# Kernel tuning notes

Hardware: AMD Instinct MI355X
Metric: run time of the kernel (lower is better)

Reference implementation:

```python
import jax, jax.numpy as jnp
import numpy as np

B, N, C = 4, 4096, 1024
H, M = 16, 64          # num_heads, num_landmarks
DH = C // H
SCALE = H ** (-0.5)    # faithful to source: num_heads**-0.5
LN_EPS = 1e-5


def setup_inputs() -> dict:
    key = jax.random.key(0)
    ks = jax.random.split(key, 8)
    s = 0.02
    return {
        "x": jax.random.normal(ks[0], (B, N, C), jnp.float32),
        "ln_w": jnp.ones((C,), jnp.float32),
        "ln_b": jnp.zeros((C,), jnp.float32),
        "qkv_w": jax.random.normal(ks[1], (3 * C, C), jnp.float32) * s,
        "qkv_b": jax.random.normal(ks[2], (3 * C,), jnp.float32) * s,
        "gamma_w": jax.random.normal(ks[3], (C, C), jnp.float32) * s,
        "gamma_b": jax.random.normal(ks[4], (C,), jnp.float32) * s,
        "proj_w": jax.random.normal(ks[5], (C, C), jnp.float32) * s,
        "proj_b": jax.random.normal(ks[6], (C,), jnp.float32) * s,
    }


def _iterative_inv(K, n_iter=6):
    # Newton-Schulz pseudo-inverse on [..., M, M]
    Id = jnp.eye(K.shape[-1], dtype=K.dtype)
    KA = jnp.abs(K)
    V0 = KA.sum(axis=-2, keepdims=True).max(axis=-1, keepdims=True)
    VI = KA.sum(axis=-1, keepdims=True).max(axis=-2, keepdims=True)
    V = jnp.swapaxes(K, -2, -1) / (V0 * VI)
    for _ in range(n_iter):
        KV = K @ V
        V = 0.25 * V @ (13.0 * Id - KV @ (15.0 * Id - KV @ (7.0 * Id - KV)))
    return V


def reference(x, ln_w, ln_b, qkv_w, qkv_b, gamma_w, gamma_b, proj_w, proj_b):
    # LayerNorm
    mu = x.mean(axis=-1, keepdims=True)
    var = x.var(axis=-1, keepdims=True)
    xn = (x - mu) * jax.lax.rsqrt(var + LN_EPS) * ln_w + ln_b
    # qkv: (B,N,3C) -> (3,B,H,N,DH)
    qkv = (xn @ qkv_w.T + qkv_b).reshape(B, N, 3, H, DH).transpose(2, 0, 3, 1, 4)
    q, k, v = qkv[0], qkv[1], qkv[2]
    # landmarks: mean-pool segments of length N//M, then scale
    q_lm = q.reshape(B, H, M, N // M, DH).mean(axis=-2) * SCALE  # (B,H,M,DH)
    k_lm = k.reshape(B, H, M, N // M, DH).mean(axis=-2) * SCALE
    attn1 = jax.nn.softmax(jnp.einsum('bhnd,bhmd->bhnm', q, k_lm), axis=-1)    # (B,H,N,M)
    attn2 = jax.nn.softmax(jnp.einsum('bhmd,bhld->bhml', q_lm, k_lm), axis=-1)  # (B,H,M,M)
    attn3 = jax.nn.softmax(jnp.einsum('bhmd,bhnd->bhmn', q_lm, k), axis=-1)    # (B,H,M,N)
    attn2_inv = _iterative_inv(attn2)
    out = attn1 @ (attn2_inv @ (attn3 @ v))            # (B,H,N,DH)
    out = out.transpose(0, 2, 1, 3).reshape(B, N, C)
    out = out @ gamma_w.T + gamma_b                    # LipNorm=True branch
    out = out @ proj_w.T + proj_b                      # proj (dropout p=0 is identity)
    return out
```

## Files before the change

kernel.cpp:

```cpp
#include <hip/hip_runtime.h>
#include <stdint.h>

typedef unsigned short u16;
typedef short bf16x8 __attribute__((ext_vector_type(8)));
typedef float f32x4 __attribute__((ext_vector_type(4)));

#define MFMA16(a, b, c) __builtin_amdgcn_mfma_f32_16x16x32_bf16((a), (b), (c), 0, 0, 0)

static __device__ __forceinline__ float bfu2f(u16 u) {
  union { unsigned int i; float f; } z; z.i = ((unsigned int)u) << 16; return z.f;
}
static __device__ __forceinline__ u16 f2bfu(float f) {
  union { float f; unsigned int i; } z; z.f = f;
  unsigned int i = z.i;
  return (u16)((i + 0x7fffu + ((i >> 16) & 1u)) >> 16);
}

__device__ __forceinline__ void gload_lds16(const void* g, void* l) {
  __builtin_amdgcn_global_load_lds((const __attribute__((address_space(1))) void*)g,
                                   (__attribute__((address_space(3))) void*)l, 16, 0, 0);
}

__global__ __launch_bounds__(256) void ln_kernel(
    const float* __restrict__ x, const float* __restrict__ w,
    const float* __restrict__ b, u16* __restrict__ xn) {
  int row = blockIdx.x;
  int t = threadIdx.x;
  const float4* xr = (const float4*)(x + (size_t)row * 1024);
  float4 v = xr[t];
  float s = v.x + v.y + v.z + v.w;
  float ss = v.x * v.x + v.y * v.y + v.z * v.z + v.w * v.w;
#pragma unroll
  for (int m = 1; m < 64; m <<= 1) { s += __shfl_xor(s, m); ss += __shfl_xor(ss, m); }
  __shared__ float sb[4], ssb[4];
  int lane = t & 63, wvi = t >> 6;
  if (lane == 0) { sb[wvi] = s; ssb[wvi] = ss; }
  __syncthreads();
  s = sb[0] + sb[1] + sb[2] + sb[3];
  ss = ssb[0] + ssb[1] + ssb[2] + ssb[3];
  float mu = s * (1.0f / 1024.0f);
  float var = ss * (1.0f / 1024.0f) - mu * mu;
  float rstd = rsqrtf(var + 1e-5f);
  float4 wv4 = ((const float4*)w)[t];
  float4 bv4 = ((const float4*)b)[t];
  ushort4 o;
  o.x = f2bfu((v.x - mu) * rstd * wv4.x + bv4.x);
  o.y = f2bfu((v.y - mu) * rstd * wv4.y + bv4.y);
  o.z = f2bfu((v.z - mu) * rstd * wv4.z + bv4.z);
  o.w = f2bfu((v.w - mu) * rstd * wv4.w + bv4.w);
  ((ushort4*)xn)[(size_t)row * 256 + t] = o;
}

__global__ void cvt3_kernel(const float* __restrict__ a, u16* __restrict__ oa, int na,
                            const float* __restrict__ b, u16* __restrict__ ob, int nb,
                            const float* __restrict__ c, u16* __restrict__ oc, int nc) {
  int total = (na + nb + nc) >> 2;
  for (int i = blockIdx.x * blockDim.x + threadIdx.x; i < total; i += gridDim.x * blockDim.x) {
    int j = i << 2;
    const float* s; u16* d; int off;
    if (j < na) { s = a; d = oa; off = j; }
    else if (j < na + nb) { s = b; d = ob; off = j - na; }
    else { s = c; d = oc; off = j - na - nb; }
    float4 v = *(const float4*)(s + off);
    ushort4 o;
    o.x = f2bfu(v.x); o.y = f2bfu(v.y); o.z = f2bfu(v.z); o.w = f2bfu(v.w);
    *(ushort4*)(d + off) = o;
  }
}

template <int MODE>
__global__ __launch_bounds__(512, 2) void gemm_bt(
    const u16* __restrict__ A, const u16* __restrict__ Bw,
    const float* __restrict__ bias,
    float* __restrict__ Cf, u16* __restrict__ Cb,
    u16* __restrict__ Qo, u16* __restrict__ Ko, u16* __restrict__ Vo,
    int M, int N, int K) {
  __shared__ __attribute__((aligned(16))) u16 As[2][16384];
  __shared__ __attribute__((aligned(16))) u16 Bs[2][16384];
  int tid = threadIdx.x;
  int lane = tid & 63;
  int w = tid >> 6;
  int wr = w >> 2, wc = w & 3;
  int r16 = lane & 15, hi = lane >> 4;
  int l8 = lane >> 3, li = lane & 7;

  int nwg = gridDim.x * gridDim.y;
  int flat = blockIdx.y * gridDim.x + blockIdx.x;
  int q8 = nwg >> 3;
  int swz = (flat & 7) * q8 + (flat >> 3);
  int bx = swz % gridDim.x, by = swz / gridDim.x;

  const char* Abase = (const char*)(A + (size_t)by * 256 * K);
  const char* Bbase = (const char*)(Bw + (size_t)bx * 256 * K);
  size_t rowbytes = (size_t)K * 2;
  int colsw = (li ^ l8) << 4;
  int nkt = K >> 6;

  f32x4 z4 = {0.f, 0.f, 0.f, 0.f};
  f32x4 acc[8][4];
#pragma unroll
  for (int m = 0; m < 8; ++m)
#pragma unroll
    for (int n = 0; n < 4; ++n) acc[m][n] = z4;

#define SG_A(buf, t, r0)                                                      \
  gload_lds16(Abase + (size_t)((r0) + w * 8 + l8) * rowbytes + ((t) << 7) +   \
                  colsw,                                                      \
              (char*)As[buf] + ((r0) + w * 8) * 128)
#define SG_B(buf, t, r0)                                                      \
  gload_lds16(Bbase + (size_t)((r0) + w * 8 + l8) * rowbytes + ((t) << 7) +   \
                  colsw,                                                      \
              (char*)Bs[buf] + ((r0) + w * 8) * 128)

  SG_A(0, 0, 0); SG_A(0, 0, 64); SG_A(0, 0, 128); SG_A(0, 0, 192);
  SG_B(0, 0, 0); SG_B(0, 0, 64); SG_B(0, 0, 128); SG_B(0, 0, 192);
  SG_A(1, 1, 0); SG_A(1, 1, 128); SG_B(1, 1, 0); SG_B(1, 1, 64);
  SG_A(1, 1, 64); SG_A(1, 1, 192);
  asm volatile("s_waitcnt vmcnt(6)" ::: "memory");
  __builtin_amdgcn_s_barrier();
  __builtin_amdgcn_sched_barrier(0);

  int buf = 0;
  bf16x8 af[4][2], bfr[4][2];

#define LDA(mh)                                                               \
  _Pragma("unroll") for (int m = 0; m < 4; ++m) {                             \
    int row = wr * 128 + (mh) * 64 + m * 16 + r16;                            \
    int sw = (row & 7) << 4;                                                  \
    _Pragma("unroll") for (int kk = 0; kk < 2; ++kk)                          \
        af[m][kk] = *(const bf16x8*)(ab + row * 128 +                         \
                                     (((kk << 6) | (hi << 4)) ^ sw));         \
  }
#define LDB(nh)                                                               \
  _Pragma("unroll") for (int n = 0; n < 2; ++n) {                             \
    int row = wc * 64 + (nh) * 32 + n * 16 + r16;                             \
    int sw = (row & 7) << 4;                                                  \
    _Pragma("unroll") for (int kk = 0; kk < 2; ++kk)                          \
        bfr[(nh) * 2 + n][kk] = *(const bf16x8*)(ab2 + row * 128 +            \
                                     (((kk << 6) | (hi << 4)) ^ sw));         \
  }
#define MM(mh, nh)                                                            \
  __builtin_amdgcn_s_setprio(1);                                              \
  _Pragma("unroll") for (int kk = 0; kk < 2; ++kk)                            \
      _Pragma("unroll") for (int m = 0; m < 4; ++m)                           \
          _Pragma("unroll") for (int n = 0; n < 2; ++n)                       \
              acc[(mh) * 4 + m][(nh) * 2 + n] =                               \
      MFMA16(af[m][kk], bfr[(nh) * 2 + n][kk], acc[(mh) * 4 + m][(nh) * 2 + n]); \
  __builtin_amdgcn_s_setprio(0)

#define BAR1                                                                  \
  __builtin_amdgcn_s_barrier();                                               \
  __builtin_amdgcn_sched_barrier(0)
#define BAR2                                                                  \
  __builtin_amdgcn_sched_barrier(0);                                          \
  __builtin_amdgcn_s_barrier();                                               \
  __builtin_amdgcn_sched_barrier(0)

  for (int t = 0; t < nkt; ++t) {
    const char* ab = (const char*)As[buf];
    const char* ab2 = (const char*)Bs[buf];
    bool s1 = (t + 1 < nkt), s2 = (t + 2 < nkt);
    LDA(0);
    LDB(0);
    if (s1) { SG_B(buf ^ 1, t + 1, 128); SG_B(buf ^ 1, t + 1, 192); }
    BAR1;
    MM(0, 0);
    BAR2;
    LDB(1);
    if (s2) { SG_A(buf, t + 2, 0); SG_A(buf, t + 2, 128); }
    BAR1;
    MM(0, 1);
    BAR2;
    LDA(1);
    if (s2) { SG_B(buf, t + 2, 0); SG_B(buf, t + 2, 64); }
    BAR1;
    MM(1, 0);
    BAR2;
    if (s2) { SG_A(buf, t + 2, 64); SG_A(buf, t + 2, 192); }
    BAR1;
    MM(1, 1);
    __builtin_amdgcn_sched_barrier(0);
    if (s2) {
      asm volatile("s_waitcnt vmcnt(6)" ::: "memory");
    } else {
      asm volatile("s_waitcnt vmcnt(0)" ::: "memory");
    }
    __builtin_amdgcn_s_barrier();
    __builtin_amdgcn_sched_barrier(0);
    buf ^= 1;
  }
#undef SG_A
#undef SG_B
#undef LDA
#undef LDB
#undef MM
#undef BAR1
#undef BAR2

#pragma unroll
  for (int m = 0; m < 8; ++m)
#pragma unroll
    for (int n = 0; n < 4; ++n) {
      int row0 = by * 256 + wr * 128 + m * 16 + hi * 4;
      int col = bx * 256 + wc * 64 + n * 16 + r16;
      if (MODE == 2) {
        int jt = col >> 10;
        int h = (col >> 6) & 15, dh = col & 63;
        int bb = row0 >> 12, nt0 = row0 & 4095;
        float bcol = bias[col];
        if (jt == 2) {
          ushort4 o;
          o.x = f2bfu(acc[m][n][0] + bcol);
          o.y = f2bfu(acc[m][n][1] + bcol);
          o.z = f2bfu(acc[m][n][2] + bcol);
          o.w = f2bfu(acc[m][n][3] + bcol);
          *(ushort4*)&Vo[(((size_t)bb * 16 + h) * 64 + dh) * 4096 + nt0] = o;
        } else {
          u16* dst = (jt == 0) ? Qo : Ko;
#pragma unroll
          for (int r = 0; r < 4; ++r)
            dst[(((size_t)bb * 16 + h) * 4096 + nt0 + r) * 64 + dh] =
                f2bfu(acc[m][n][r] + bcol);
        }
      } else {
        float bcol = bias[col];
#pragma unroll
        for (int r = 0; r < 4; ++r) {
          int row = row0 + r;
          float val = acc[m][n][r] + bcol;
          if (MODE == 1) Cf[(size_t)row * N + col] = val;
          else           Cb[(size_t)row * N + col] = f2bfu(val);
        }
      }
    }
}

__global__ __launch_bounds__(256) void w2_kernel(
    const u16* __restrict__ A, const u16* __restrict__ Bw,
    float* __restrict__ Cp) {
  __shared__ __attribute__((aligned(16))) u16 As[8192];
  __shared__ __attribute__((aligned(16))) u16 Bs[8192];
  int tid = threadIdx.x, lane = tid & 63, w = tid >> 6;
  int wr = w >> 1, wc = w & 1;
  int r16 = lane & 15, hi = lane >> 4;
  int l8 = lane >> 3, li = lane & 7;
  int bx = blockIdx.x, by = blockIdx.y, kz = blockIdx.z;
  const char* Abase = (const char*)(A + (size_t)by * 131072 + kz * 256);
  const char* Bbase = (const char*)(Bw + (size_t)bx * 131072 + kz * 256);
  int colsw = (li ^ l8) << 4;
  f32x4 z4 = {0.f, 0.f, 0.f, 0.f};
  f32x4 acc[4][4];
#pragma unroll
  for (int m = 0; m < 4; ++m)
#pragma unroll
    for (int n = 0; n < 4; ++n) acc[m][n] = z4;

  for (int kt = 0; kt < 4; ++kt) {
    int kb = kt << 7;
#pragma unroll
    for (int i = 0; i < 4; ++i) {
      int c = w * 4 + i;
      int rr = c * 8 + l8;
      gload_lds16(Abase + (size_t)rr * 2048 + kb + colsw, (char*)As + c * 1024);
      gload_lds16(Bbase + (size_t)rr * 2048 + kb + colsw, (char*)Bs + c * 1024);
    }
    __syncthreads();
    int sw = (lane & 7) << 4;
#pragma unroll
    for (int kk = 0; kk < 2; ++kk) {
      int kby = (kk << 6) + (hi << 4);
      bf16x8 af[4], bfr[4];
#pragma unroll
      for (int m = 0; m < 4; ++m) {
        int row = wr * 64 + m * 16 + r16;
        af[m] = *(const bf16x8*)((const char*)As + row * 128 + (kby ^ sw));
      }
#pragma unroll
      for (int n = 0; n < 4; ++n) {
        int row = wc * 64 + n * 16 + r16;
        bfr[n] = *(const bf16x8*)((const char*)Bs + row * 128 + (kby ^ sw));
      }
#pragma unroll
      for (int m = 0; m < 4; ++m)
#pragma unroll
        for (int n = 0; n < 4; ++n) acc[m][n] = MFMA16(af[m], bfr[n], acc[m][n]);
    }
    __syncthreads();
  }
#pragma unroll
  for (int m = 0; m < 4; ++m)
#pragma unroll
    for (int n = 0; n < 4; ++n)
#pragma unroll
      for (int r = 0; r < 4; ++r) {
        int row = by * 128 + wr * 64 + m * 16 + hi * 4 + r;
        int col = bx * 128 + wc * 64 + n * 16 + r16;
        Cp[(size_t)kz * 1048576 + (size_t)row * 1024 + col] = acc[m][n][r];
      }
}

__global__ __launch_bounds__(256) void w2_reduce_kernel(
    const float* __restrict__ Cp, u16* __restrict__ W2b) {
  int idx4 = blockIdx.x * 256 + threadIdx.x;
  const float4* p = (const float4*)Cp + idx4;
  float4 s = p[0];
  float4 b = p[262144], c = p[524288], d = p[786432];
  s.x += b.x + c.x + d.x;
  s.y += b.y + c.y + d.y;
  s.z += b.z + c.z + d.z;
  s.w += b.w + c.w + d.w;
  ushort4 o;
  o.x = f2bfu(s.x); o.y = f2bfu(s.y); o.z = f2bfu(s.z); o.w = f2bfu(s.w);
  ((ushort4*)W2b)[idx4] = o;
}

__global__ __launch_bounds__(64) void landmark_kernel(
    const u16* __restrict__ Q, const u16* __restrict__ K,
    float* __restrict__ qlmf, u16* __restrict__ qlmb,
    float* __restrict__ klmf, u16* __restrict__ klmb) {
  int bm = blockIdx.x;
  int bh = bm >> 6, m = bm & 63;
  int l = threadIdx.x;
  const u16* src = blockIdx.y ? K : Q;
  const u16* base = src + (((size_t)bh * 4096) + m * 64) * 64;
  int r0 = l >> 3;
  int c0 = (l & 7) * 8;
  float s[8] = {};
#pragma unroll
  for (int p = 0; p < 8; ++p) {
    bf16x8 v = *(const bf16x8*)(base + (size_t)(r0 + p * 8) * 64 + c0);
#pragma unroll
    for (int j = 0; j < 8; ++j) s[j] += bfu2f((u16)v[j]);
  }
#pragma unroll
  for (int j = 0; j < 8; ++j) {
    s[j] += __shfl_xor(s[j], 8);
    s[j] += __shfl_xor(s[j], 16);
    s[j] += __shfl_xor(s[j], 32);
  }
  if (l < 8) {
    size_t o = (size_t)bh * 4096 + m * 64 + l * 8;
    float* fo = blockIdx.y ? klmf : qlmf;
    u16* bo = blockIdx.y ? klmb : qlmb;
#pragma unroll
    for (int j = 0; j < 8; ++j) {
      float val = s[j] * (0.25f / 64.0f);
      fo[o + j] = val;
      bo[o + j] = f2bfu(val);
    }
  }
}

__global__ __launch_bounds__(256) void attn3_pv_kernel(
    const u16* __restrict__ qlmb, const u16* __restrict__ Kmat,
    const u16* __restrict__ Vt, float* __restrict__ Upart,
    float* __restrict__ rspart) {
  __shared__ __attribute__((aligned(16))) u16 Elds[4][8192];
  int chunk = blockIdx.x, bh = blockIdx.y;
  int tid = threadIdx.x, lane = tid & 63, w = tid >> 6;
  int r16 = lane & 15, hi = lane >> 4;
  int keybase = chunk * 512 + w * 128;
  const u16* kb = Kmat + ((size_t)bh * 4096 + keybase) * 64;
  const u16* vtb = Vt + (size_t)bh * 262144;
  const u16* qb = qlmb + (size_t)bh * 4096;
  u16* eb = &Elds[w][0];
  f32x4 z4 = {0.f, 0.f, 0.f, 0.f};

  bf16x8 afr[4][2];
#pragma unroll
  for (int m = 0; m < 4; ++m)
#pragma unroll
    for (int kk = 0; kk < 2; ++kk)
      afr[m][kk] = *(const bf16x8*)(qb + (m * 16 + r16) * 64 + kk * 32 + hi * 8);

  float rs[4][4] = {};
  for (int cf = 0; cf < 8; ++cf) {
    f32x4 S[4] = {z4, z4, z4, z4};
#pragma unroll
    for (int kk = 0; kk < 2; ++kk) {
      bf16x8 bfr = *(const bf16x8*)(kb + (size_t)(cf * 16 + r16) * 64 + kk * 32 + hi * 8);
#pragma unroll
      for (int m = 0; m < 4; ++m) S[m] = MFMA16(afr[m][kk], bfr, S[m]);
    }
#pragma unroll
    for (int m = 0; m < 4; ++m)
#pragma unroll
      for (int r = 0; r < 4; ++r) {
        float e = __expf(S[m][r]);
        rs[m][r] += e;
        int row = m * 16 + hi * 4 + r;
        int key = cf * 16 + r16;
        *(u16*)((char*)eb + row * 256 + ((key * 2) ^ ((row & 7) << 4))) = f2bfu(e);
      }
  }
#pragma unroll
  for (int m = 0; m < 4; ++m)
#pragma unroll
    for (int r = 0; r < 4; ++r) {
      float v = rs[m][r];
      v += __shfl_xor(v, 1); v += __shfl_xor(v, 2);
      v += __shfl_xor(v, 4); v += __shfl_xor(v, 8);
      rs[m][r] = v;
    }
  if (r16 == 0) {
    float* rp = rspart + (((size_t)bh * 8 + chunk) * 4 + w) * 64;
#pragma unroll
    for (int m = 0; m < 4; ++m)
#pragma unroll
      for (int r = 0; r < 4; ++r) rp[m * 16 + hi * 4 + r] = rs[m][r];
  }
  __syncthreads();

  f32x4 U[4][4];
#pragma unroll
  for (int m = 0; m < 4; ++m)
#pragma unroll
    for (int df = 0; df < 4; ++df) U[m][df] = z4;
  for (int ks = 0; ks < 4; ++ks) {
    bf16x8 ea[4];
#pragma unroll
    for (int m = 0; m < 4; ++m) {
      int row = m * 16 + r16;
      ea[m] = *(const bf16x8*)((char*)eb + row * 256 + (((ks * 32 + hi * 8) * 2) ^ ((row & 7) << 4)));
    }
#pragma unroll
    for (int df = 0; df < 4; ++df) {
      bf16x8 vb8 = *(const bf16x8*)(vtb + (size_t)(df * 16 + r16) * 4096 +
                                    keybase + ks * 32 + hi * 8);
#pragma unroll
      for (int m = 0; m < 4; ++m) U[m][df] = MFMA16(ea[m], vb8, U[m][df]);
    }
  }
  float* up = Upart + (((size_t)bh * 8 + chunk) * 4 + w) * 4096;
#pragma unroll
  for (int m = 0; m < 4; ++m)
#pragma unroll
    for (int df = 0; df < 4; ++df)
#pragma unroll
      for (int r = 0; r < 4; ++r)
        up[(m * 16 + hi * 4 + r) * 64 + df * 16 + r16] = U[m][df][r];
}

__global__ __launch_bounds__(256) void reduce_t_kernel(
    const float* __restrict__ Upart, const float* __restrict__ rspart,
    float* __restrict__ Tmf) {
  int bh = blockIdx.y;
  int tid = threadIdx.x;
  __shared__ float rsum[64];
  if (tid < 64) {
    float s = 0.f;
    const float* rp = rspart + (size_t)bh * 2048 + tid;
#pragma unroll 8
    for (int p = 0; p < 32; ++p) s += rp[p * 64];
    rsum[tid] = s;
  }
  __syncthreads();
  int idx4 = blockIdx.x * 256 + tid;
  const float4* up = (const float4*)(Upart + (size_t)bh * 131072) + idx4;
  float4 s = {0.f, 0.f, 0.f, 0.f};
#pragma unroll 8
  for (int p = 0; p < 32; ++p) {
    float4 v = up[p * 1024];
    s.x += v.x; s.y += v.y; s.z += v.z; s.w += v.w;
  }
  float inv = 1.0f / rsum[idx4 >> 4];
  s.x *= inv; s.y *= inv; s.z *= inv; s.w *= inv;
  ((float4*)(Tmf + (size_t)bh * 4096))[idx4] = s;
}

__global__ __launch_bounds__(256) void transpose_g_kernel(
    const float* __restrict__ G, u16* __restrict__ GT) {
  __shared__ float t[64][65];
  int tr = blockIdx.y * 64, tc = blockIdx.x * 64;
  int l = threadIdx.x & 63, y = threadIdx.x >> 6;
  for (int r = y; r < 64; r += 4)
    t[r][l] = G[(size_t)(tr + r) * 1024 + tc + l];
  __syncthreads();
  for (int rr = y; rr < 64; rr += 4)
    GT[(size_t)(tc + rr) * 1024 + tr + l] = f2bfu(t[l][rr]);
}

__global__ __launch_bounds__(256) void bias2_kernel(
    const float* __restrict__ P, const float* __restrict__ gb,
    const float* __restrict__ pb, float* __restrict__ b2) {
  int i = blockIdx.x * 256 + threadIdx.x;
  const float4* pr = (const float4*)(P + (size_t)i * 1024);
  const float4* g4 = (const float4*)gb;
  float s = 0.f;
  for (int k = 0; k < 256; ++k) {
    float4 a = pr[k], b = g4[k];
    s += a.x * b.x + a.y * b.y + a.z * b.z + a.w * b.w;
  }
  b2[i] = s + pb[i];
}

__device__ __forceinline__ void mm64d(const float (*AT)[68], const float (*Bm)[68],
                                      float (*C)[68], float (*CT)[68],
                                      float alpha, float dconst, bool dmode,
                                      int tid) {
  int tr = (tid >> 4) << 2;
  int tc = (tid & 15) << 2;
  float acc[4][4] = {};
#pragma unroll 4
  for (int k = 0; k < 64; ++k) {
    float4 av = *(const float4*)&AT[k][tr];
    float4 bv = *(const float4*)&Bm[k][tc];
    float aa[4] = {av.x, av.y, av.z, av.w};
    float bb[4] = {bv.x, bv.y, bv.z, bv.w};
#pragma unroll
    for (int i = 0; i < 4; ++i)
#pragma unroll
      for (int j = 0; j < 4; ++j) acc[i][j] = fmaf(aa[i], bb[j], acc[i][j]);
  }
#pragma unroll
  for (int i = 0; i < 4; ++i)
#pragma unroll
    for (int j = 0; j < 4; ++j) {
      float raw = acc[i][j] * alpha;
      if (CT) CT[tc + j][tr + i] = raw;
      C[tr + i][tc + j] =
          dmode ? (((tr + i) == (tc + j)) ? dconst - raw : -raw) : raw;
    }
}

__global__ __launch_bounds__(256) void combine_ns_kernel(
    const float* __restrict__ Tmf, const float* __restrict__ qlmf,
    const float* __restrict__ klmf, u16* __restrict__ WT) {
  __shared__ __attribute__((aligned(16))) float A2T[64][68];
  __shared__ __attribute__((aligned(16))) float Vv[64][68];
  __shared__ __attribute__((aligned(16))) float VT[64][68];
  __shared__ __attribute__((aligned(16))) float KV[64][68];
  __shared__ __attribute__((aligned(16))) float KVT[64][68];
  __shared__ __attribute__((aligned(16))) float T2[64][68];
  __shared__ __attribute__((aligned(16))) float T4[64][68];
  __shared__ __attribute__((aligned(16))) float Tm[64][68];
  __shared__ float redbuf[64];
  __shared__ float v0s, scal;
  int bh = blockIdx.x, tid = threadIdx.x;

  for (int idx = tid; idx < 1024; idx += 256) {
    float4 v = ((const float4*)(Tmf + (size_t)bh * 4096))[idx];
    int r = idx >> 4, c0 = (idx & 15) << 2;
    *(float4*)&Tm[r][c0] = v;
  }
  for (int idx = tid; idx < 4096; idx += 256) {
    int r = idx >> 6, c = idx & 63;
    Vv[c][r] = qlmf[(size_t)bh * 4096 + idx];
    VT[c][r] = klmf[(size_t)bh * 4096 + idx];
  }
  __syncthreads();
  mm64d(&Vv[0], &VT[0], &T2[0], nullptr, 1.0f, 0.f, false, tid);
  __syncthreads();
  if (tid < 64) {
    float mx = -1e30f;
    for (int c2 = 0; c2 < 64; ++c2) mx = fmaxf(mx, T2[tid][c2]);
    float s = 0.f;
    for (int c2 = 0; c2 < 64; ++c2) { float e = __expf(T2[tid][c2] - mx); T2[tid][c2] = e; s += e; }
    float inv = 1.f / s;
    for (int c2 = 0; c2 < 64; ++c2) { float p = T2[tid][c2] * inv; T2[tid][c2] = p; A2T[c2][tid] = p; }
  }
  __syncthreads();
  if (tid < 64) {
    float cs = 0.f;
    for (int r2 = 0; r2 < 64; ++r2) cs += fabsf(T2[r2][tid]);
    redbuf[tid] = cs;
  }
  __syncthreads();
  if (tid == 0) {
    float v0 = 0.f;
    for (int c2 = 0; c2 < 64; ++c2) v0 = fmaxf(v0, redbuf[c2]);
    v0s = v0;
  }
  __syncthreads();
  if (tid < 64) {
    float rs2 = 0.f;
    for (int c2 = 0; c2 < 64; ++c2) rs2 += fabsf(T2[tid][c2]);
    redbuf[tid] = rs2;
  }
  __syncthreads();
  if (tid == 0) {
    float vi = 0.f;
    for (int r2 = 0; r2 < 64; ++r2) vi = fmaxf(vi, redbuf[r2]);
    scal = 1.0f / (v0s * vi);
  }
  __syncthreads();
  for (int idx = tid; idx < 4096; idx += 256) {
    int r = idx >> 6, c = idx & 63;
    Vv[r][c] = A2T[r][c] * scal;
    VT[r][c] = T2[r][c] * scal;
  }
  __syncthreads();
  float (*Vt_r)[68] = VT;
  float (*Vt_w)[68] = KV;
#pragma unroll 1
  for (int it = 0; it < 6; ++it) {
    mm64d(&A2T[0], &Vv[0], &T2[0], &KVT[0], 1.0f, 7.0f, true, tid);
    __syncthreads();
    mm64d(&KVT[0], &T2[0], &T4[0], nullptr, 1.0f, 15.0f, true, tid);
    __syncthreads();
    mm64d(&KVT[0], &T4[0], &T2[0], nullptr, 1.0f, 13.0f, true, tid);
    __syncthreads();
    mm64d(Vt_r, &T2[0], &Vv[0], Vt_w, 0.25f, 0.f, false, tid);
    __syncthreads();
    float (*tmp)[68] = Vt_r; Vt_r = Vt_w; Vt_w = tmp;
  }
  mm64d(Vt_r, &Tm[0], &T2[0], nullptr, 1.0f, 0.f, false, tid);
  __syncthreads();
  for (int idx = tid; idx < 4096; idx += 256) {
    int r = idx >> 6, c = idx & 63;
    WT[(size_t)bh * 4096 + c * 64 + r] = f2bfu(T2[r][c]);
  }
}

__global__ __launch_bounds__(256) void attn1_out_kernel(
    const u16* __restrict__ Q, const u16* __restrict__ klmb,
    const u16* __restrict__ WT, u16* __restrict__ AO) {
  __shared__ __attribute__((aligned(16))) u16 Elds[4][2048];
  int bh = blockIdx.y;
  int b = bh >> 4, h = bh & 15;
  int tid = threadIdx.x, lane = tid & 63, w = tid >> 6;
  int r16 = lane & 15, hi = lane >> 4;
  int rowbase = blockIdx.x * 128 + w * 32;
  const u16* qb = Q + ((size_t)bh * 4096 + rowbase) * 64;
  const u16* kb = klmb + (size_t)bh * 4096;
  const u16* wtb = WT + (size_t)bh * 4096;
  u16* eb = &Elds[w][0];
  f32x4 z4 = {0.f, 0.f, 0.f, 0.f};

  bf16x8 afr[2][2];
#pragma unroll
  for (int mi = 0; mi < 2; ++mi)
#pragma unroll
    for (int kk = 0; kk < 2; ++kk)
      afr[mi][kk] = *(const bf16x8*)(qb + (mi * 16 + r16) * 64 + kk * 32 + hi * 8);

  float rs[2][4] = {};
  for (int cf = 0; cf < 4; ++cf) {
    f32x4 S[2] = {z4, z4};
#pragma unroll
    for (int kk = 0; kk < 2; ++kk) {
      bf16x8 bfr = *(const bf16x8*)(kb + (cf * 16 + r16) * 64 + kk * 32 + hi * 8);
#pragma unroll
      for (int mi = 0; mi < 2; ++mi) S[mi] = MFMA16(afr[mi][kk], bfr, S[mi]);
    }
#pragma unroll
    for (int mi = 0; mi < 2; ++mi)
#pragma unroll
      for (int r = 0; r < 4; ++r) {
        float e = __expf(S[mi][r]);
        rs[mi][r] += e;
        int row = mi * 16 + hi * 4 + r;
        int key = cf * 16 + r16;
        *(u16*)((char*)eb + row * 128 + ((key * 2) ^ ((row & 7) << 4))) = f2bfu(e);
      }
  }
#pragma unroll
  for (int mi = 0; mi < 2; ++mi)
#pragma unroll
    for (int r = 0; r < 4; ++r) {
      float v = rs[mi][r];
      v += __shfl_xor(v, 1); v += __shfl_xor(v, 2);
      v += __shfl_xor(v, 4); v += __shfl_xor(v, 8);
      rs[mi][r] = v;
    }
  __syncthreads();

  f32x4 O[2][4];
#pragma unroll
  for (int mi = 0; mi < 2; ++mi)
#pragma unroll
    for (int df = 0; df < 4; ++df) O[mi][df] = z4;
  for (int ks = 0; ks < 2; ++ks) {
    bf16x8 ea[2];
#pragma unroll
    for (int mi = 0; mi < 2; ++mi) {
      int row = mi * 16 + r16;
      ea[mi] = *(const bf16x8*)((char*)eb + row * 128 + (((ks * 32 + hi * 8) * 2) ^ ((row & 7) << 4)));
    }
#pragma unroll
    for (int df = 0; df < 4; ++df) {
      bf16x8 wfr = *(const bf16x8*)(wtb + (df * 16 + r16) * 64 + ks * 32 + hi * 8);
#pragma unroll
      for (int mi = 0; mi < 2; ++mi) O[mi][df] = MFMA16(ea[mi], wfr, O[mi][df]);
    }
  }
#pragma unroll
  for (int mi = 0; mi < 2; ++mi)
#pragma unroll
    for (int df = 0; df < 4; ++df)
#pragma unroll
      for (int r = 0; r < 4; ++r) {
        int row = mi * 16 + hi * 4 + r;
        int n = rowbase + row;
        int col = h * 64 + df * 16 + r16;
        float val = O[mi][df][r] / rs[mi][r];
        AO[((size_t)b * 4096 + n) * 1024 + col] = f2bfu(val);
      }
}

extern "C" void kernel_launch(void* const* d_in, const int* in_sizes, int n_in,
                              void* d_out, int out_size, void* d_ws, size_t ws_size,
                              hipStream_t stream) {
  (void)in_sizes; (void)n_in; (void)out_size; (void)ws_size;
  const float* x       = (const float*)d_in[0];
  const float* ln_w    = (const float*)d_in[1];
  const float* ln_b    = (const float*)d_in[2];
  const float* qkv_w   = (const float*)d_in[3];
  const float* qkv_b   = (const float*)d_in[4];
  const float* gamma_w = (const float*)d_in[5];
  const float* gamma_b = (const float*)d_in[6];
  const float* proj_w  = (const float*)d_in[7];
  const float* proj_b  = (const float*)d_in[8];

  char* ws = (char*)d_ws;
  u16* XN     = (u16*)(ws + 0);
  u16* Qb     = (u16*)(ws + 33554432);
  u16* Kb     = (u16*)(ws + 67108864);
  u16* Vb     = (u16*)(ws + 100663296);
  u16* QKVW   = (u16*)(ws + 134217728);
  u16* GW     = (u16*)(ws + 140509184);
  u16* PW     = (u16*)(ws + 142606336);
  float* QLMF = (float*)(ws + 144703488);
  float* KLMF = (float*)(ws + 145752064);
  u16* QLMB   = (u16*)(ws + 146800640);
  u16* KLMB   = (u16*)(ws + 147324928);
  float* RSP  = (float*)(ws + 147849216);
  u16* WTb    = (u16*)(ws + 148373504);
  float* UP   = (float*)XN;
  float* TMF  = (float*)Kb;
  u16* GTb    = (u16*)(ws + 100663296);
  u16* W2b    = (u16*)(ws + 102760448);
  float* B2F  = (float*)(ws + 104857600);
  float* CPF  = (float*)(ws + 109051904);

  ln_kernel<<<16384, 256, 0, stream>>>(x, ln_w, ln_b, XN);
  cvt3_kernel<<<2048, 256, 0, stream>>>(qkv_w, QKVW, 3145728,
                                        gamma_w, GW, 1048576,
                                        proj_w, PW, 1048576);
  gemm_bt<2><<<dim3(12, 64), 512, 0, stream>>>(XN, QKVW, qkv_b, nullptr, nullptr,
                                               Qb, Kb, Vb, 16384, 3072, 1024);
  landmark_kernel<<<dim3(4096, 2), 64, 0, stream>>>(Qb, Kb, QLMF, QLMB, KLMF, KLMB);
  attn3_pv_kernel<<<dim3(8, 64), 256, 0, stream>>>(QLMB, Kb, Vb, UP, RSP);
  reduce_t_kernel<<<dim3(4, 64), 256, 0, stream>>>(UP, RSP, TMF);
  transpose_g_kernel<<<dim3(16, 16), 256, 0, stream>>>(gamma_w, GTb);
  w2_kernel<<<dim3(8, 8, 4), 256, 0, stream>>>(PW, GTb, CPF);
  w2_reduce_kernel<<<1024, 256, 0, stream>>>(CPF, W2b);
  bias2_kernel<<<4, 256, 0, stream>>>(proj_w, gamma_b, proj_b, B2F);
  combine_ns_kernel<<<64, 256, 0, stream>>>(TMF, QLMF, KLMF, WTb);
  attn1_out_kernel<<<dim3(32, 64), 256, 0, stream>>>(Qb, KLMB, WTb, XN);
  gemm_bt<1><<<dim3(4, 64), 512, 0, stream>>>(XN, W2b, B2F, (float*)d_out, nullptr,
                                              nullptr, nullptr, nullptr, 16384, 1024, 1024);
}
```

Baseline: 377.4 us.

## Merge prep kernels, fold bias into reduce, batch attn3 chunks, reorder GEMM LDS loads

LayerNorm, weight conversion and the gamma transpose are merged into one prep kernel, and the bias2 computation is folded into w2_reduce, which cuts the number of launches. The gamma_w bf16 conversion is dropped because the transpose already produces the bf16 copy that is used. attn3_pv now processes two 512-key batches per block, halving the grid and the partial buffers that reduce_t must sum. In the GEMM main loop the next LDS fragment loads are issued before the barrier, so they overlap the MFMA work. The costs are fewer blocks in attn3_pv and possible divergence across block types in the merged kernels.

New measurement: 371.0 us. About the same (-1.7%).

```diff
diff --git a/kernel.cpp b/kernel.cpp
--- a/kernel.cpp
+++ b/kernel.cpp
@@ -21,50 +21,61 @@
                                    (__attribute__((address_space(3))) void*)l, 16, 0, 0);
 }
 
-__global__ __launch_bounds__(256) void ln_kernel(
-    const float* __restrict__ x, const float* __restrict__ w,
-    const float* __restrict__ b, u16* __restrict__ xn) {
-  int row = blockIdx.x;
+__global__ __launch_bounds__(256) void prep_kernel(
+    const float* __restrict__ x, const float* __restrict__ lw,
+    const float* __restrict__ lb, u16* __restrict__ xn,
+    const float* __restrict__ qkvw, u16* __restrict__ QKVW,
+    const float* __restrict__ projw, u16* __restrict__ PW,
+    const float* __restrict__ G, u16* __restrict__ GT) {
+  int blk = blockIdx.x;
   int t = threadIdx.x;
-  const float4* xr = (const float4*)(x + (size_t)row * 1024);
-  float4 v = xr[t];
-  float s = v.x + v.y + v.z + v.w;
-  float ss = v.x * v.x + v.y * v.y + v.z * v.z + v.w * v.w;
-#pragma unroll
-  for (int m = 1; m < 64; m <<= 1) { s += __shfl_xor(s, m); ss += __shfl_xor(ss, m); }
-  __shared__ float sb[4], ssb[4];
-  int lane = t & 63, wvi = t >> 6;
-  if (lane == 0) { sb[wvi] = s; ssb[wvi] = ss; }
-  __syncthreads();
-  s = sb[0] + sb[1] + sb[2] + sb[3];
-  ss = ssb[0] + ssb[1] + ssb[2] + ssb[3];
-  float mu = s * (1.0f / 1024.0f);
-  float var = ss * (1.0f / 1024.0f) - mu * mu;
-  float rstd = rsqrtf(var + 1e-5f);
-  float4 wv4 = ((const float4*)w)[t];
-  float4 bv4 = ((const float4*)b)[t];
-  ushort4 o;
-  o.x = f2bfu((v.x - mu) * rstd * wv4.x + bv4.x);
-  o.y = f2bfu((v.y - mu) * rstd * wv4.y + bv4.y);
-  o.z = f2bfu((v.z - mu) * rstd * wv4.z + bv4.z);
-  o.w = f2bfu((v.w - mu) * rstd * wv4.w + bv4.w);
-  ((ushort4*)xn)[(size_t)row * 256 + t] = o;
-}
-
-__global__ void cvt3_kernel(const float* __restrict__ a, u16* __restrict__ oa, int na,
-                            const float* __restrict__ b, u16* __restrict__ ob, int nb,
-                            const float* __restrict__ c, u16* __restrict__ oc, int nc) {
-  int total = (na + nb + nc) >> 2;
-  for (int i = blockIdx.x * blockDim.x + threadIdx.x; i < total; i += gridDim.x * blockDim.x) {
-    int j = i << 2;
-    const float* s; u16* d; int off;
-    if (j < na) { s = a; d = oa; off = j; }
-    else if (j < na + nb) { s = b; d = ob; off = j - na; }
-    else { s = c; d = oc; off = j - na - nb; }
-    float4 v = *(const float4*)(s + off);
+  if (blk < 16384) {
+    int row = blk;
+    const float4* xr = (const float4*)(x + (size_t)row * 1024);
+    float4 v = xr[t];
+    float s = v.x + v.y + v.z + v.w;
+    float ss = v.x * v.x + v.y * v.y + v.z * v.z + v.w * v.w;
+#pragma unroll
+    for (int m = 1; m < 64; m <<= 1) { s += __shfl_xor(s, m); ss += __shfl_xor(ss, m); }
+    __shared__ float sb[4], ssb[4];
+    int lane = t & 63, wvi = t >> 6;
+    if (lane == 0) { sb[wvi] = s; ssb[wvi] = ss; }
+    __syncthreads();
+    s = sb[0] + sb[1] + sb[2] + sb[3];
+    ss = ssb[0] + ssb[1] + ssb[2] + ssb[3];
+    float mu = s * (1.0f / 1024.0f);
+    float var = ss * (1.0f / 1024.0f) - mu * mu;
+    float rstd = rsqrtf(var + 1e-5f);
+    float4 wv4 = ((const float4*)lw)[t];
+    float4 bv4 = ((const float4*)lb)[t];
     ushort4 o;
-    o.x = f2bfu(v.x); o.y = f2bfu(v.y); o.z = f2bfu(v.z); o.w = f2bfu(v.w);
-    *(ushort4*)(d + off) = o;
+    o.x = f2bfu((v.x - mu) * rstd * wv4.x + bv4.x);
+    o.y = f2bfu((v.y - mu) * rstd * wv4.y + bv4.y);
+    o.z = f2bfu((v.z - mu) * rstd * wv4.z + bv4.z);
+    o.w = f2bfu((v.w - mu) * rstd * wv4.w + bv4.w);
+    ((ushort4*)xn)[(size_t)row * 256 + t] = o;
+  } else if (blk < 18432) {
+    int idx = (blk - 16384) * 256 + t;
+    for (int i = idx; i < 1048576; i += 524288) {
+      int j = i << 2;
+      const float* s2; u16* d; int off;
+      if (j < 3145728) { s2 = qkvw; d = QKVW; off = j; }
+      else             { s2 = projw; d = PW; off = j - 3145728; }
+      float4 v = *(const float4*)(s2 + off);
+      ushort4 o;
+      o.x = f2bfu(v.x); o.y = f2bfu(v.y); o.z = f2bfu(v.z); o.w = f2bfu(v.w);
+      *(ushort4*)(d + off) = o;
+    }
+  } else {
+    __shared__ float tt[64][65];
+    int tg = blk - 18432;
+    int tr = (tg >> 4) * 64, tc = (tg & 15) * 64;
+    int l = t & 63, y = t >> 6;
+    for (int r = y; r < 64; r += 4)
+      tt[r][l] = G[(size_t)(tr + r) * 1024 + tc + l];
+    __syncthreads();
+    for (int rr = y; rr < 64; rr += 4)
+      GT[(size_t)(tc + rr) * 1024 + tr + l] = f2bfu(tt[l][rr]);
   }
 }
 
@@ -148,13 +159,14 @@
       MFMA16(af[m][kk], bfr[(nh) * 2 + n][kk], acc[(mh) * 4 + m][(nh) * 2 + n]); \
   __builtin_amdgcn_s_setprio(0)
 
+#define SBAR __builtin_amdgcn_sched_barrier(0)
 #define BAR1                                                                  \
   __builtin_amdgcn_s_barrier();                                               \
-  __builtin_amdgcn_sched_barrier(0)
+  SBAR
 #define BAR2                                                                  \
-  __builtin_amdgcn_sched_barrier(0);                                          \
+  SBAR;                                                                       \
   __builtin_amdgcn_s_barrier();                                               \
-  __builtin_amdgcn_sched_barrier(0)
+  SBAR
 
   for (int t = 0; t < nkt; ++t) {
     const char* ab = (const char*)As[buf];
@@ -165,13 +177,15 @@
     if (s1) { SG_B(buf ^ 1, t + 1, 128); SG_B(buf ^ 1, t + 1, 192); }
     BAR1;
     MM(0, 0);
+    SBAR;
+    LDB(1);
     BAR2;
-    LDB(1);
     if (s2) { SG_A(buf, t + 2, 0); SG_A(buf, t + 2, 128); }
     BAR1;
     MM(0, 1);
+    SBAR;
+    LDA(1);
     BAR2;
-    LDA(1);
     if (s2) { SG_B(buf, t + 2, 0); SG_B(buf, t + 2, 64); }
     BAR1;
     MM(1, 0);
@@ -179,14 +193,14 @@
     if (s2) { SG_A(buf, t + 2, 64); SG_A(buf, t + 2, 192); }
     BAR1;
     MM(1, 1);
-    __builtin_amdgcn_sched_barrier(0);
+    SBAR;
     if (s2) {
       asm volatile("s_waitcnt vmcnt(6)" ::: "memory");
     } else {
       asm volatile("s_waitcnt vmcnt(0)" ::: "memory");
     }
     __builtin_amdgcn_s_barrier();
-    __builtin_amdgcn_sched_barrier(0);
+    SBAR;
     buf ^= 1;
   }
 #undef SG_A
@@ -196,6 +210,7 @@
 #undef MM
 #undef BAR1
 #undef BAR2
+#undef SBAR
 
 #pragma unroll
   for (int m = 0; m < 8; ++m)
@@ -227,9 +242,7 @@
 #pragma unroll
         for (int r = 0; r < 4; ++r) {
           int row = row0 + r;
-          float val = acc[m][n][r] + bcol;
-          if (MODE == 1) Cf[(size_t)row * N + col] = val;
-          else           Cb[(size_t)row * N + col] = f2bfu(val);
+          Cf[(size_t)row * N + col] = acc[m][n][r] + bcol;
         }
       }
     }
@@ -300,18 +313,32 @@
 }
 
 __global__ __launch_bounds__(256) void w2_reduce_kernel(
-    const float* __restrict__ Cp, u16* __restrict__ W2b) {
-  int idx4 = blockIdx.x * 256 + threadIdx.x;
-  const float4* p = (const float4*)Cp + idx4;
-  float4 s = p[0];
-  float4 b = p[262144], c = p[524288], d = p[786432];
-  s.x += b.x + c.x + d.x;
-  s.y += b.y + c.y + d.y;
-  s.z += b.z + c.z + d.z;
-  s.w += b.w + c.w + d.w;
-  ushort4 o;
-  o.x = f2bfu(s.x); o.y = f2bfu(s.y); o.z = f2bfu(s.z); o.w = f2bfu(s.w);
-  ((ushort4*)W2b)[idx4] = o;
+    const float* __restrict__ Cp, u16* __restrict__ W2b,
+    const float* __restrict__ P, const float* __restrict__ gb,
+    const float* __restrict__ pb, float* __restrict__ b2) {
+  if (blockIdx.x < 1024) {
+    int idx4 = blockIdx.x * 256 + threadIdx.x;
+    const float4* p = (const float4*)Cp + idx4;
+    float4 s = p[0];
+    float4 b = p[262144], c = p[524288], d = p[786432];
+    s.x += b.x + c.x + d.x;
+    s.y += b.y + c.y + d.y;
+    s.z += b.z + c.z + d.z;
+    s.w += b.w + c.w + d.w;
+    ushort4 o;
+    o.x = f2bfu(s.x); o.y = f2bfu(s.y); o.z = f2bfu(s.z); o.w = f2bfu(s.w);
+    ((ushort4*)W2b)[idx4] = o;
+  } else {
+    int i = (blockIdx.x - 1024) * 256 + threadIdx.x;
+    const float4* pr = (const float4*)(P + (size_t)i * 1024);
+    const float4* g4 = (const float4*)gb;
+    float s = 0.f;
+    for (int k = 0; k < 256; ++k) {
+      float4 a = pr[k], b = g4[k];
+      s += a.x * b.x + a.y * b.y + a.z * b.z + a.w * b.w;
+    }
+    b2[i] = s + pb[i];
+  }
 }
 
 __global__ __launch_bounds__(64) void landmark_kernel(
@@ -359,8 +386,6 @@
   int chunk = blockIdx.x, bh = blockIdx.y;
   int tid = threadIdx.x, lane = tid & 63, w = tid >> 6;
   int r16 = lane & 15, hi = lane >> 4;
-  int keybase = chunk * 512 + w * 128;
-  const u16* kb = Kmat + ((size_t)bh * 4096 + keybase) * 64;
   const u16* vtb = Vt + (size_t)bh * 262144;
   const u16* qb = qlmb + (size_t)bh * 4096;
   u16* eb = &Elds[w][0];
@@ -374,25 +399,53 @@
       afr[m][kk] = *(const bf16x8*)(qb + (m * 16 + r16) * 64 + kk * 32 + hi * 8);
 
   float rs[4][4] = {};
-  for (int cf = 0; cf < 8; ++cf) {
-    f32x4 S[4] = {z4, z4, z4, z4};
-#pragma unroll
-    for (int kk = 0; kk < 2; ++kk) {
-      bf16x8 bfr = *(const bf16x8*)(kb + (size_t)(cf * 16 + r16) * 64 + kk * 32 + hi * 8);
-#pragma unroll
-      for (int m = 0; m < 4; ++m) S[m] = MFMA16(afr[m][kk], bfr, S[m]);
-    }
-#pragma unroll
-    for (int m = 0; m < 4; ++m)
-#pragma unroll
-      for (int r = 0; r < 4; ++r) {
-        float e = __expf(S[m][r]);
-        rs[m][r] += e;
-        int row = m * 16 + hi * 4 + r;
-        int key = cf * 16 + r16;
-        *(u16*)((char*)eb + row * 256 + ((key * 2) ^ ((row & 7) << 4))) = f2bfu(e);
-      }
-  }
+  f32x4 U[4][4];
+#pragma unroll
+  for (int m = 0; m < 4; ++m)
+#pragma unroll
+    for (int df = 0; df < 4; ++df) U[m][df] = z4;
+
+  for (int bat = 0; bat < 2; ++bat) {
+    int keybase = chunk * 1024 + bat * 512 + w * 128;
+    const u16* kb = Kmat + ((size_t)bh * 4096 + keybase) * 64;
+    for (int cf = 0; cf < 8; ++cf) {
+      f32x4 S[4] = {z4, z4, z4, z4};
+#pragma unroll
+      for (int kk = 0; kk < 2; ++kk) {
+        bf16x8 bfr = *(const bf16x8*)(kb + (size_t)(cf * 16 + r16) * 64 + kk * 32 + hi * 8);
+#pragma unroll
+        for (int m = 0; m < 4; ++m) S[m] = MFMA16(afr[m][kk], bfr, S[m]);
+      }
+#pragma unroll
+      for (int m = 0; m < 4; ++m)
+#pragma unroll
+        for (int r = 0; r < 4; ++r) {
+          float e = __expf(S[m][r]);
+          rs[m][r] += e;
+          int row = m * 16 + hi * 4 + r;
+          int key = cf * 16 + r16;
+          *(u16*)((char*)eb + row * 256 + ((key * 2) ^ ((row & 7) << 4))) = f2bfu(e);
+        }
+    }
+    __syncthreads();
+    for (int ks = 0; ks < 4; ++ks) {
+      bf16x8 ea[4];
+#pragma unroll
+      for (int m = 0; m < 4; ++m) {
+        int row = m * 16 + r16;
+        ea[m] = *(const bf16x8*)((char*)eb + row * 256 + (((ks * 32 + hi * 8) * 2) ^ ((row & 7) << 4)));
+      }
+#pragma unroll
+      for (int df = 0; df < 4; ++df) {
+        bf16x8 vb8 = *(const bf16x8*)(vtb + (size_t)(df * 16 + r16) * 4096 +
+                                      keybase + ks * 32 + hi * 8);
+#pragma unroll
+        for (int m = 0; m < 4; ++m) U[m][df] = MFMA16(ea[m], vb8, U[m][df]);
+      }
+    }
+    __syncthreads();
+  }
+
 #pragma unroll
   for (int m = 0; m < 4; ++m)
 #pragma unroll
@@ -403,35 +456,13 @@
       rs[m][r] = v;
     }
   if (r16 == 0) {
-    float* rp = rspart + (((size_t)bh * 8 + chunk) * 4 + w) * 64;
+    float* rp = rspart + (((size_t)bh * 4 + chunk) * 4 + w) * 64;
 #pragma unroll
     for (int m = 0; m < 4; ++m)
 #pragma unroll
       for (int r = 0; r < 4; ++r) rp[m * 16 + hi * 4 + r] = rs[m][r];
   }
-  __syncthreads();
-
-  f32x4 U[4][4];
-#pragma unroll
-  for (int m = 0; m < 4; ++m)
-#pragma unroll
-    for (int df = 0; df < 4; ++df) U[m][df] = z4;
-  for (int ks = 0; ks < 4; ++ks) {
-    bf16x8 ea[4];
-#pragma unroll
-    for (int m = 0; m < 4; ++m) {
-      int row = m * 16 + r16;
-      ea[m] = *(const bf16x8*)((char*)eb + row * 256 + (((ks * 32 + hi * 8) * 2) ^ ((row & 7) << 4)));
-    }
-#pragma unroll
-    for (int df = 0; df < 4; ++df) {
-      bf16x8 vb8 = *(const bf16x8*)(vtb + (size_t)(df * 16 + r16) * 4096 +
-                                    keybase + ks * 32 + hi * 8);
-#pragma unroll
-      for (int m = 0; m < 4; ++m) U[m][df] = MFMA16(ea[m], vb8, U[m][df]);
-    }
-  }
-  float* up = Upart + (((size_t)bh * 8 + chunk) * 4 + w) * 4096;
+  float* up = Upart + (((size_t)bh * 4 + chunk) * 4 + w) * 4096;
 #pragma unroll
   for (int m = 0; m < 4; ++m)
 #pragma unroll
@@ -449,49 +480,23 @@
   __shared__ float rsum[64];
   if (tid < 64) {
     float s = 0.f;
-    const float* rp = rspart + (size_t)bh * 2048 + tid;
+    const float* rp = rspart + (size_t)bh * 1024 + tid;
 #pragma unroll 8
-    for (int p = 0; p < 32; ++p) s += rp[p * 64];
+    for (int p = 0; p < 16; ++p) s += rp[p * 64];
     rsum[tid] = s;
   }
   __syncthreads();
   int idx4 = blockIdx.x * 256 + tid;
-  const float4* up = (const float4*)(Upart + (size_t)bh * 131072) + idx4;
+  const float4* up = (const float4*)(Upart + (size_t)bh * 65536) + idx4;
   float4 s = {0.f, 0.f, 0.f, 0.f};
 #pragma unroll 8
-  for (int p = 0; p < 32; ++p) {
+  for (int p = 0; p < 16; ++p) {
     float4 v = up[p * 1024];
     s.x += v.x; s.y += v.y; s.z += v.z; s.w += v.w;
   }
   float inv = 1.0f / rsum[idx4 >> 4];
   s.x *= inv; s.y *= inv; s.z *= inv; s.w *= inv;
   ((float4*)(Tmf + (size_t)bh * 4096))[idx4] = s;
-}
-
-__global__ __launch_bounds__(256) void transpose_g_kernel(
-    const float* __restrict__ G, u16* __restrict__ GT) {
-  __shared__ float t[64][65];
-  int tr = blockIdx.y * 64, tc = blockIdx.x * 64;
-  int l = threadIdx.x & 63, y = threadIdx.x >> 6;
-  for (int r = y; r < 64; r += 4)
-    t[r][l] = G[(size_t)(tr + r) * 1024 + tc + l];
-  __syncthreads();
-  for (int rr = y; rr < 64; rr += 4)
-    GT[(size_t)(tc + rr) * 1024 + tr + l] = f2bfu(t[l][rr]);
-}
-
-__global__ __launch_bounds__(256) void bias2_kernel(
-    const float* __restrict__ P, const float* __restrict__ gb,
-    const float* __restrict__ pb, float* __restrict__ b2) {
-  int i = blockIdx.x * 256 + threadIdx.x;
-  const float4* pr = (const float4*)(P + (size_t)i * 1024);
-  const float4* g4 = (const float4*)gb;
-  float s = 0.f;
-  for (int k = 0; k < 256; ++k) {
-    float4 a = pr[k], b = g4[k];
-    s += a.x * b.x + a.y * b.y + a.z * b.z + a.w * b.w;
-  }
-  b2[i] = s + pb[i];
 }
 
 __device__ __forceinline__ void mm64d(const float (*AT)[68], const float (*Bm)[68],
@@ -718,7 +723,7 @@
   u16* Kb     = (u16*)(ws + 67108864);
   u16* Vb     = (u16*)(ws + 100663296);
   u16* QKVW   = (u16*)(ws + 134217728);
-  u16* GW     = (u16*)(ws + 140509184);
+  u16* GTb    = (u16*)(ws + 140509184);
   u16* PW     = (u16*)(ws + 142606336);
   float* QLMF = (float*)(ws + 144703488);
   float* KLMF = (float*)(ws + 145752064);
@@ -727,25 +732,20 @@
   float* RSP  = (float*)(ws + 147849216);
   u16* WTb    = (u16*)(ws + 148373504);
   float* UP   = (float*)XN;
+  float* CPF  = (float*)(ws + 16777216);
   float* TMF  = (float*)Kb;
-  u16* GTb    = (u16*)(ws + 100663296);
   u16* W2b    = (u16*)(ws + 102760448);
   float* B2F  = (float*)(ws + 104857600);
-  float* CPF  = (float*)(ws + 109051904);
-
-  ln_kernel<<<16384, 256, 0, stream>>>(x, ln_w, ln_b, XN);
-  cvt3_kernel<<<2048, 256, 0, stream>>>(qkv_w, QKVW, 3145728,
-                                        gamma_w, GW, 1048576,
-                                        proj_w, PW, 1048576);
+
+  prep_kernel<<<18688, 256, 0, stream>>>(x, ln_w, ln_b, XN,
+                                         qkv_w, QKVW, proj_w, PW, gamma_w, GTb);
   gemm_bt<2><<<dim3(12, 64), 512, 0, stream>>>(XN, QKVW, qkv_b, nullptr, nullptr,
                                                Qb, Kb, Vb, 16384, 3072, 1024);
   landmark_kernel<<<dim3(4096, 2), 64, 0, stream>>>(Qb, Kb, QLMF, QLMB, KLMF, KLMB);
-  attn3_pv_kernel<<<dim3(8, 64), 256, 0, stream>>>(QLMB, Kb, Vb, UP, RSP);
+  attn3_pv_kernel<<<dim3(4, 64), 256, 0, stream>>>(QLMB, Kb, Vb, UP, RSP);
   reduce_t_kernel<<<dim3(4, 64), 256, 0, stream>>>(UP, RSP, TMF);
-  transpose_g_kernel<<<dim3(16, 16), 256, 0, stream>>>(gamma_w, GTb);
   w2_kernel<<<dim3(8, 8, 4), 256, 0, stream>>>(PW, GTb, CPF);
-  w2_reduce_kernel<<<1024, 256, 0, stream>>>(CPF, W2b);
-  bias2_kernel<<<4, 256, 0, stream>>>(proj_w, gamma_b, proj_b, B2F);
+  w2_reduce_kernel<<<1028, 256, 0, stream>>>(CPF, W2b, proj_w, gamma_b, proj_b, B2F);
   combine_ns_kernel<<<64, 256, 0, stream>>>(TMF, QLMF, KLMF, WTb);
   attn1_out_kernel<<<dim3(32, 64), 256, 0, stream>>>(Qb, KLMB, WTb, XN);
   gemm_bt<1><<<dim3(4, 64), 512, 0, stream>>>(XN, W2b, B2F, (float*)d_out, nullptr,
```
